# Optimization experiments

Measured on AMD Instinct MI355X. Metric: run time of the kernel, lower is better.

## Reference

```python
import jax, jax.numpy as jnp
import numpy as np

T, TOPK = 512, 2
E, H, D = 8, 2816, 1024


def setup_inputs() -> dict:
    key = jax.random.key(0)
    k1, k2, k3, k4, k5 = jax.random.split(key, 5)
    x = jax.random.normal(k1, (T, D), dtype=jnp.float32)
    expert_indices = jax.random.randint(k2, (T, TOPK), 0, E, dtype=jnp.int64)
    w1 = jax.random.normal(k3, (E, H, D), dtype=jnp.float32)
    w2 = jax.random.normal(k4, (E, H, D), dtype=jnp.float32)
    w3 = jax.random.normal(k5, (E, H, D), dtype=jnp.float32)
    return {"x": x, "expert_indices": expert_indices, "w1": w1, "w2": w2, "w3": w3}


def reference(x, expert_indices, w1, w2, w3):
    # Math identical to: silu(x @ w1[e].T) * (x @ w3[e].T) @ w2[e] for e = expert_indices[t, a].
    # Computed densely over all experts (GEMM-friendly), then gathered per token,
    # which avoids materializing [T, a, H, D] gathered weight tensors.
    h1 = jax.nn.silu(jnp.einsum('ti,ehi->teh', x, w1))   # [T, E, H]
    h3 = jnp.einsum('ti,ehi->teh', x, w3)                # [T, E, H]
    out_all = jnp.einsum('teh,ehi->tei', h1 * h3, w2)    # [T, E, D]
    # gather the top_k selected experts per token -> [T, TOPK, D]
    idx = expert_indices[:, :, None]                     # [T, a, 1]
    expert_outs = jnp.take_along_axis(out_all, idx, axis=1)
    return expert_outs
```

## Files before the change

kernel.cpp:

```cpp
#include <hip/hip_runtime.h>


#define NEXP 8
#define HDIM 2816
#define DDIM 1024
#define NPAIR 1024

typedef unsigned int uint;
typedef unsigned short ushort;
typedef __attribute__((ext_vector_type(8))) short bf16x8;
typedef __attribute__((ext_vector_type(4))) float fvec4;
typedef __attribute__((ext_vector_type(4))) uint uvec4;
typedef __attribute__((ext_vector_type(2))) uint uvec2;

__device__ __forceinline__ ushort f2bf(float f) {
    uint u = __builtin_bit_cast(uint, f);
    u += 0x7fff + ((u >> 16) & 1);
    return (ushort)(u >> 16);
}
__device__ __forceinline__ uint pack2(float lo, float hi) {
    return (uint)f2bf(lo) | ((uint)f2bf(hi) << 16);
}

__global__ __launch_bounds__(1024) void route_kernel(const int* __restrict__ idx,
                                                     int* __restrict__ counts,
                                                     int* __restrict__ lists) {
    int p = threadIdx.x;
    if (p < NEXP) counts[p] = 0;
    __syncthreads();
    int e = idx[p];
    int pos = atomicAdd(&counts[e], 1);
    lists[e * NPAIR + pos] = p;
}

#define LDA1 36

__global__ __launch_bounds__(512) void h_mfma(const float* __restrict__ x,
                       const float* __restrict__ w1,
                       const float* __restrict__ w3,
                       const int* __restrict__ counts,
                       const int* __restrict__ lists,
                       ushort* __restrict__ hb) {
    const int e = blockIdx.x;
    const int cnt = counts[e];
    const int m0 = blockIdx.z * 128;
    if (m0 >= cnt) return;
    const int h0 = blockIdx.y * 64;

    __shared__ ushort sA[128 * LDA1];
    __shared__ ushort sB1[64 * LDA1];
    __shared__ ushort sB3[64 * LDA1];
    __shared__ int sTok[128];
    __shared__ int sPairS[128];

    const int tid = threadIdx.x;
    if (tid < 128) {
        int m = m0 + tid;
        int mc = (m < cnt) ? m : (cnt - 1);
        int p = lists[e * NPAIR + mc];
        sTok[tid] = p >> 1;
        sPairS[tid] = (m < cnt) ? p : -1;
    }
    __syncthreads();

    const int w = tid >> 6;
    const int lane = tid & 63;
    const int l16 = lane & 15;
    const int quad = lane >> 4;

    const int arow = tid >> 3;
    const int ac4  = tid & 7;

    fvec4 acc1[4], acc3[4];
    #pragma unroll
    for (int i = 0; i < 4; ++i) { acc1[i] = (fvec4)0.f; acc3[i] = (fvec4)0.f; }

    const float* w1e = w1 + (size_t)e * HDIM * DDIM + (size_t)h0 * DDIM;
    const float* w3e = w3 + (size_t)e * HDIM * DDIM + (size_t)h0 * DDIM;
    const float* xr0 = x + (size_t)sTok[arow] * DDIM + ac4 * 4;
    const float* xr1 = x + (size_t)sTok[arow + 64] * DDIM + ac4 * 4;
    const float* wr1 = w1e + (size_t)arow * DDIM + ac4 * 4;
    const float* wr3 = w3e + (size_t)arow * DDIM + ac4 * 4;

    fvec4 va0, va1, vb1, vb3;
    va0 = *(const fvec4*)(xr0);
    va1 = *(const fvec4*)(xr1);
    vb1 = *(const fvec4*)(wr1);
    vb3 = *(const fvec4*)(wr3);

    for (int k0 = 0; k0 < DDIM; k0 += 32) {
        __syncthreads();
        {
            uvec2 t;
            t = (uvec2){ pack2(va0[0], va0[1]), pack2(va0[2], va0[3]) };
            *(uvec2*)&sA[arow * LDA1 + ac4 * 4] = t;
            t = (uvec2){ pack2(va1[0], va1[1]), pack2(va1[2], va1[3]) };
            *(uvec2*)&sA[(arow + 64) * LDA1 + ac4 * 4] = t;
            t = (uvec2){ pack2(vb1[0], vb1[1]), pack2(vb1[2], vb1[3]) };
            *(uvec2*)&sB1[arow * LDA1 + ac4 * 4] = t;
            t = (uvec2){ pack2(vb3[0], vb3[1]), pack2(vb3[2], vb3[3]) };
            *(uvec2*)&sB3[arow * LDA1 + ac4 * 4] = t;
        }
        __syncthreads();

        int kn = (k0 + 32 < DDIM) ? (k0 + 32) : k0;
        va0 = *(const fvec4*)(xr0 + kn);
        va1 = *(const fvec4*)(xr1 + kn);
        vb1 = *(const fvec4*)(wr1 + kn);
        vb3 = *(const fvec4*)(wr3 + kn);

        bf16x8 af = *(const bf16x8*)&sA[(w * 16 + l16) * LDA1 + quad * 8];
        #pragma unroll
        for (int ni = 0; ni < 4; ++ni) {
            bf16x8 b1 = *(const bf16x8*)&sB1[(ni * 16 + l16) * LDA1 + quad * 8];
            bf16x8 b3 = *(const bf16x8*)&sB3[(ni * 16 + l16) * LDA1 + quad * 8];
            acc1[ni] = __builtin_amdgcn_mfma_f32_16x16x32_bf16(af, b1, acc1[ni], 0, 0, 0);
            acc3[ni] = __builtin_amdgcn_mfma_f32_16x16x32_bf16(af, b3, acc3[ni], 0, 0, 0);
        }
    }

    #pragma unroll
    for (int r = 0; r < 4; ++r) {
        int m = w * 16 + quad * 4 + r;
        int p = sPairS[m];
        if (p >= 0) {
            size_t base = (size_t)p * HDIM + h0;
            #pragma unroll
            for (int ni = 0; ni < 4; ++ni) {
                float a = acc1[ni][r];
                float g = acc3[ni][r];
                float s = a / (1.f + __expf(-a)) * g;
                hb[base + ni * 16 + l16] = f2bf(s);
            }
        }
    }
}

#define LDA2 68

__global__ __launch_bounds__(512) void out_mfma(const float* __restrict__ w2,
                         const int* __restrict__ counts,
                         const int* __restrict__ lists,
                         const ushort* __restrict__ hb,
                         float* __restrict__ out) {
    const int e = blockIdx.x;
    const int cnt = counts[e];
    const int mb = blockIdx.z >> 2;
    const int sk = blockIdx.z & 3;
    const int m0 = mb * 128;
    if (m0 >= cnt) return;
    const int n0 = blockIdx.y * 64;
    const int kbase = sk * (HDIM / 4);

    __shared__ ushort sA[128 * LDA2];
    __shared__ ushort sB[64 * LDA2];
    __shared__ int sPairC[128];
    __shared__ int sPairS[128];

    const int tid = threadIdx.x;
    if (tid < 128) {
        int m = m0 + tid;
        int mc = (m < cnt) ? m : (cnt - 1);
        int p = lists[e * NPAIR + mc];
        sPairC[tid] = p;
        sPairS[tid] = (m < cnt) ? p : -1;
    }
    __syncthreads();

    const int w = tid >> 6;
    const int lane = tid & 63;
    const int l16 = lane & 15;
    const int quad = lane >> 4;

    const int arow = tid >> 3;
    const int ac   = tid & 7;
    const int kp   = tid >> 4;
    const int n4   = tid & 15;

    fvec4 acc[4];
    #pragma unroll
    for (int i = 0; i < 4; ++i) acc[i] = (fvec4)0.f;

    const float* w2e = w2 + (size_t)e * HDIM * DDIM + n0;
    const ushort* ha0 = hb + (size_t)sPairC[arow] * HDIM + ac * 8;
    const ushort* ha1 = hb + (size_t)sPairC[arow + 64] * HDIM + ac * 8;
    const float* wk0 = w2e + (size_t)(kbase + 2 * kp) * DDIM + n4 * 4;

    uvec4 va0, va1;
    fvec4 fa, fb;
    va0 = *(const uvec4*)(ha0 + kbase);
    va1 = *(const uvec4*)(ha1 + kbase);
    fa = *(const fvec4*)(wk0);
    fb = *(const fvec4*)(wk0 + DDIM);

    const int NCH = (HDIM / 4) / 64;
    for (int kc = 0; kc < NCH; ++kc) {
        __syncthreads();
        *(uvec4*)&sA[arow * LDA2 + ac * 8] = va0;
        *(uvec4*)&sA[(arow + 64) * LDA2 + ac * 8] = va1;
        #pragma unroll
        for (int j = 0; j < 4; ++j)
            *(uint*)&sB[(n4 * 4 + j) * LDA2 + kp * 2] = pack2(fa[j], fb[j]);
        __syncthreads();

        int kcn = (kc + 1 < NCH) ? (kc + 1) : kc;
        int koff = kcn * 64;
        va0 = *(const uvec4*)(ha0 + kbase + koff);
        va1 = *(const uvec4*)(ha1 + kbase + koff);
        fa = *(const fvec4*)(wk0 + (size_t)koff * DDIM);
        fb = *(const fvec4*)(wk0 + (size_t)(koff + 1) * DDIM);

        #pragma unroll
        for (int kk = 0; kk < 64; kk += 32) {
            bf16x8 af = *(const bf16x8*)&sA[(w * 16 + l16) * LDA2 + kk + quad * 8];
            #pragma unroll
            for (int ni = 0; ni < 4; ++ni) {
                bf16x8 bf = *(const bf16x8*)&sB[(ni * 16 + l16) * LDA2 + kk + quad * 8];
                acc[ni] = __builtin_amdgcn_mfma_f32_16x16x32_bf16(af, bf, acc[ni], 0, 0, 0);
            }
        }
    }

    #pragma unroll
    for (int r = 0; r < 4; ++r) {
        int m = w * 16 + quad * 4 + r;
        int p = sPairS[m];
        if (p >= 0) {
            #pragma unroll
            for (int ni = 0; ni < 4; ++ni)
                atomicAdd(&out[(size_t)p * DDIM + n0 + ni * 16 + l16], acc[ni][r]);
        }
    }
}

extern "C" void kernel_launch(void* const* d_in, const int* in_sizes, int n_in,
                              void* d_out, int out_size, void* d_ws, size_t ws_size,
                              hipStream_t stream) {
    const float* x   = (const float*)d_in[0];
    const int*   idx = (const int*)d_in[1];
    const float* w1  = (const float*)d_in[2];
    const float* w2  = (const float*)d_in[3];
    const float* w3  = (const float*)d_in[4];
    float* out = (float*)d_out;

    char* ws = (char*)d_ws;
    int*    counts = (int*)ws;
    int*    lists  = (int*)(ws + 1024);
    ushort* hbuf   = (ushort*)(ws + 65536);

    hipMemsetAsync(out, 0, (size_t)out_size * sizeof(float), stream);
    route_kernel<<<1, NPAIR, 0, stream>>>(idx, counts, lists);
    h_mfma<<<dim3(NEXP, HDIM / 64, NPAIR / 128), 512, 0, stream>>>(
        x, w1, w3, counts, lists, hbuf);
    out_mfma<<<dim3(NEXP, DDIM / 64, (NPAIR / 128) * 4), 512, 0, stream>>>(
        w2, counts, lists, hbuf, out);
}
```

Baseline: 322.9 us.

## Double-buffer weight tiles in LDS and load activation fragments directly from global

Both GEMM kernels drop the LDS staging of the A operand (gathered x rows or hidden rows). Each wave now loads its MFMA A fragments straight from global memory into registers. Weight tiles are staged as bf16 in double-buffered LDS with a 64-wide K chunk and a two-chunk-deep register prefetch, so only one barrier is needed per chunk instead of two. Launch bounds now request 3 blocks per CU. The aim is to cut barrier stalls and LDS traffic and overlap global loads with MFMA work, at the cost of more registers and A loads that are less coalesced.

```diff
diff --git a/kernel.cpp b/kernel.cpp
--- a/kernel.cpp
+++ b/kernel.cpp
@@ -11,7 +11,6 @@
 typedef __attribute__((ext_vector_type(8))) short bf16x8;
 typedef __attribute__((ext_vector_type(4))) float fvec4;
 typedef __attribute__((ext_vector_type(4))) uint uvec4;
-typedef __attribute__((ext_vector_type(2))) uint uvec2;
 
 __device__ __forceinline__ ushort f2bf(float f) {
     uint u = __builtin_bit_cast(uint, f);
@@ -20,6 +19,19 @@
 }
 __device__ __forceinline__ uint pack2(float lo, float hi) {
     return (uint)f2bf(lo) | ((uint)f2bf(hi) << 16);
+}
+__device__ __forceinline__ uvec4 pack8(fvec4 a, fvec4 b) {
+    uvec4 v;
+    v.x = pack2(a.x, a.y); v.y = pack2(a.z, a.w);
+    v.z = pack2(b.x, b.y); v.w = pack2(b.z, b.w);
+    return v;
+}
+
+__device__ __forceinline__ void wg_sync_lds() {
+    __builtin_amdgcn_sched_barrier(0);
+    asm volatile("s_waitcnt lgkmcnt(0)" ::: "memory");
+    __builtin_amdgcn_s_barrier();
+    __builtin_amdgcn_sched_barrier(0);
 }
 
 __global__ __launch_bounds__(1024) void route_kernel(const int* __restrict__ idx,
@@ -33,9 +45,10 @@
     lists[e * NPAIR + pos] = p;
 }
 
-#define LDA1 36
-
-__global__ __launch_bounds__(512) void h_mfma(const float* __restrict__ x,
+#define LDB 68
+#define NCH1 (DDIM / 64)
+
+__global__ __launch_bounds__(512, 3) void h_mfma(const float* __restrict__ x,
                        const float* __restrict__ w1,
                        const float* __restrict__ w3,
                        const int* __restrict__ counts,
@@ -47,9 +60,8 @@
     if (m0 >= cnt) return;
     const int h0 = blockIdx.y * 64;
 
-    __shared__ ushort sA[128 * LDA1];
-    __shared__ ushort sB1[64 * LDA1];
-    __shared__ ushort sB3[64 * LDA1];
+    __shared__ ushort sB1[2][64 * LDB];
+    __shared__ ushort sB3[2][64 * LDB];
     __shared__ int sTok[128];
     __shared__ int sPairS[128];
 
@@ -61,62 +73,73 @@
         sTok[tid] = p >> 1;
         sPairS[tid] = (m < cnt) ? p : -1;
     }
-    __syncthreads();
 
     const int w = tid >> 6;
     const int lane = tid & 63;
     const int l16 = lane & 15;
     const int quad = lane >> 4;
 
-    const int arow = tid >> 3;
-    const int ac4  = tid & 7;
+    const int brow = tid >> 3;
+    const int bc = (tid & 7) * 8;
+    const float* pB1 = w1 + (size_t)e * HDIM * DDIM + (size_t)(h0 + brow) * DDIM + bc;
+    const float* pB3 = w3 + (size_t)e * HDIM * DDIM + (size_t)(h0 + brow) * DDIM + bc;
+
+    fvec4 pf[2][4];
+
+#define P1_ISSUE(S, KC) do { \
+    const float* q1 = pB1 + (KC) * 64; \
+    const float* q3 = pB3 + (KC) * 64; \
+    pf[S][0] = *(const fvec4*)q1;  pf[S][1] = *(const fvec4*)(q1 + 4); \
+    pf[S][2] = *(const fvec4*)q3;  pf[S][3] = *(const fvec4*)(q3 + 4); \
+} while (0)
+
+#define P1_STAGE(S, B) do { \
+    *(uvec4*)&sB1[B][brow * LDB + bc] = pack8(pf[S][0], pf[S][1]); \
+    *(uvec4*)&sB3[B][brow * LDB + bc] = pack8(pf[S][2], pf[S][3]); \
+} while (0)
+
+    P1_ISSUE(0, 0);
+    P1_ISSUE(1, 1);
+    wg_sync_lds();
+    const float* xA = x + (size_t)sTok[w * 16 + l16] * DDIM + quad * 8;
 
     fvec4 acc1[4], acc3[4];
     #pragma unroll
     for (int i = 0; i < 4; ++i) { acc1[i] = (fvec4)0.f; acc3[i] = (fvec4)0.f; }
 
-    const float* w1e = w1 + (size_t)e * HDIM * DDIM + (size_t)h0 * DDIM;
-    const float* w3e = w3 + (size_t)e * HDIM * DDIM + (size_t)h0 * DDIM;
-    const float* xr0 = x + (size_t)sTok[arow] * DDIM + ac4 * 4;
-    const float* xr1 = x + (size_t)sTok[arow + 64] * DDIM + ac4 * 4;
-    const float* wr1 = w1e + (size_t)arow * DDIM + ac4 * 4;
-    const float* wr3 = w3e + (size_t)arow * DDIM + ac4 * 4;
-
-    fvec4 va0, va1, vb1, vb3;
-    va0 = *(const fvec4*)(xr0);
-    va1 = *(const fvec4*)(xr1);
-    vb1 = *(const fvec4*)(wr1);
-    vb3 = *(const fvec4*)(wr3);
-
-    for (int k0 = 0; k0 < DDIM; k0 += 32) {
-        __syncthreads();
-        {
-            uvec2 t;
-            t = (uvec2){ pack2(va0[0], va0[1]), pack2(va0[2], va0[3]) };
-            *(uvec2*)&sA[arow * LDA1 + ac4 * 4] = t;
-            t = (uvec2){ pack2(va1[0], va1[1]), pack2(va1[2], va1[3]) };
-            *(uvec2*)&sA[(arow + 64) * LDA1 + ac4 * 4] = t;
-            t = (uvec2){ pack2(vb1[0], vb1[1]), pack2(vb1[2], vb1[3]) };
-            *(uvec2*)&sB1[arow * LDA1 + ac4 * 4] = t;
-            t = (uvec2){ pack2(vb3[0], vb3[1]), pack2(vb3[2], vb3[3]) };
-            *(uvec2*)&sB3[arow * LDA1 + ac4 * 4] = t;
-        }
-        __syncthreads();
-
-        int kn = (k0 + 32 < DDIM) ? (k0 + 32) : k0;
-        va0 = *(const fvec4*)(xr0 + kn);
-        va1 = *(const fvec4*)(xr1 + kn);
-        vb1 = *(const fvec4*)(wr1 + kn);
-        vb3 = *(const fvec4*)(wr3 + kn);
-
-        bf16x8 af = *(const bf16x8*)&sA[(w * 16 + l16) * LDA1 + quad * 8];
-        #pragma unroll
-        for (int ni = 0; ni < 4; ++ni) {
-            bf16x8 b1 = *(const bf16x8*)&sB1[(ni * 16 + l16) * LDA1 + quad * 8];
-            bf16x8 b3 = *(const bf16x8*)&sB3[(ni * 16 + l16) * LDA1 + quad * 8];
-            acc1[ni] = __builtin_amdgcn_mfma_f32_16x16x32_bf16(af, b1, acc1[ni], 0, 0, 0);
-            acc3[ni] = __builtin_amdgcn_mfma_f32_16x16x32_bf16(af, b3, acc3[ni], 0, 0, 0);
-        }
+    P1_STAGE(0, 0);
+    wg_sync_lds();
+
+#define P1_BODY(T, CUR) do { \
+    const int kA = (T) * 64; \
+    fvec4 a0 = *(const fvec4*)(xA + kA); \
+    fvec4 a1 = *(const fvec4*)(xA + kA + 4); \
+    fvec4 a2 = *(const fvec4*)(xA + kA + 32); \
+    fvec4 a3 = *(const fvec4*)(xA + kA + 36); \
+    if ((T) + 2 < NCH1) P1_ISSUE(CUR, (T) + 2); \
+    bf16x8 af0 = __builtin_bit_cast(bf16x8, pack8(a0, a1)); \
+    bf16x8 af1 = __builtin_bit_cast(bf16x8, pack8(a2, a3)); \
+    _Pragma("unroll") \
+    for (int ni = 0; ni < 4; ++ni) { \
+        const int ro = (ni * 16 + l16) * LDB + quad * 8; \
+        bf16x8 b10 = *(const bf16x8*)&sB1[CUR][ro]; \
+        bf16x8 b30 = *(const bf16x8*)&sB3[CUR][ro]; \
+        bf16x8 b11 = *(const bf16x8*)&sB1[CUR][ro + 32]; \
+        bf16x8 b31 = *(const bf16x8*)&sB3[CUR][ro + 32]; \
+        acc1[ni] = __builtin_amdgcn_mfma_f32_16x16x32_bf16(af0, b10, acc1[ni], 0, 0, 0); \
+        acc3[ni] = __builtin_amdgcn_mfma_f32_16x16x32_bf16(af0, b30, acc3[ni], 0, 0, 0); \
+        acc1[ni] = __builtin_amdgcn_mfma_f32_16x16x32_bf16(af1, b11, acc1[ni], 0, 0, 0); \
+        acc3[ni] = __builtin_amdgcn_mfma_f32_16x16x32_bf16(af1, b31, acc3[ni], 0, 0, 0); \
+    } \
+    if ((T) + 1 < NCH1) { \
+        P1_STAGE(CUR ^ 1, CUR ^ 1); \
+        wg_sync_lds(); \
+    } \
+} while (0)
+
+    for (int t = 0; t < NCH1; t += 2) {
+        P1_BODY(t, 0);
+        P1_BODY(t + 1, 1);
     }
 
     #pragma unroll
@@ -136,9 +159,10 @@
     }
 }
 
-#define LDA2 68
-
-__global__ __launch_bounds__(512) void out_mfma(const float* __restrict__ w2,
+#define LDB2 68
+#define NCH2 ((HDIM / 4) / 64)
+
+__global__ __launch_bounds__(512, 3) void out_mfma(const float* __restrict__ w2,
                          const int* __restrict__ counts,
                          const int* __restrict__ lists,
                          const ushort* __restrict__ hb,
@@ -152,8 +176,7 @@
     const int n0 = blockIdx.y * 64;
     const int kbase = sk * (HDIM / 4);
 
-    __shared__ ushort sA[128 * LDA2];
-    __shared__ ushort sB[64 * LDA2];
+    __shared__ ushort sB[2][64 * LDB2];
     __shared__ int sPairC[128];
     __shared__ int sPairS[128];
 
@@ -165,60 +188,65 @@
         sPairC[tid] = p;
         sPairS[tid] = (m < cnt) ? p : -1;
     }
-    __syncthreads();
 
     const int w = tid >> 6;
     const int lane = tid & 63;
     const int l16 = lane & 15;
     const int quad = lane >> 4;
-
-    const int arow = tid >> 3;
-    const int ac   = tid & 7;
-    const int kp   = tid >> 4;
-    const int n4   = tid & 15;
+    const int kp = tid >> 4;
+    const int n4 = tid & 15;
+
+    const float* pW = w2 + (size_t)e * HDIM * DDIM
+                         + (size_t)(kbase + 2 * kp) * DDIM + n0 + n4 * 4;
+
+    fvec4 pw[2][2];
+
+#define P2_ISSUE(S, KC) do { \
+    const float* q = pW + (size_t)(KC) * 64 * DDIM; \
+    pw[S][0] = *(const fvec4*)q; \
+    pw[S][1] = *(const fvec4*)(q + DDIM); \
+} while (0)
+
+#define P2_STAGE(S, B) do { \
+    _Pragma("unroll") \
+    for (int j = 0; j < 4; ++j) \
+        *(uint*)&sB[B][(n4 * 4 + j) * LDB2 + kp * 2] = pack2(pw[S][0][j], pw[S][1][j]); \
+} while (0)
+
+    P2_ISSUE(0, 0);
+    P2_ISSUE(1, 1);
+    wg_sync_lds();
+    const ushort* pA = hb + (size_t)sPairC[w * 16 + l16] * HDIM + kbase + quad * 8;
 
     fvec4 acc[4];
     #pragma unroll
     for (int i = 0; i < 4; ++i) acc[i] = (fvec4)0.f;
 
-    const float* w2e = w2 + (size_t)e * HDIM * DDIM + n0;
-    const ushort* ha0 = hb + (size_t)sPairC[arow] * HDIM + ac * 8;
-    const ushort* ha1 = hb + (size_t)sPairC[arow + 64] * HDIM + ac * 8;
-    const float* wk0 = w2e + (size_t)(kbase + 2 * kp) * DDIM + n4 * 4;
-
-    uvec4 va0, va1;
-    fvec4 fa, fb;
-    va0 = *(const uvec4*)(ha0 + kbase);
-    va1 = *(const uvec4*)(ha1 + kbase);
-    fa = *(const fvec4*)(wk0);
-    fb = *(const fvec4*)(wk0 + DDIM);
-
-    const int NCH = (HDIM / 4) / 64;
-    for (int kc = 0; kc < NCH; ++kc) {
-        __syncthreads();
-        *(uvec4*)&sA[arow * LDA2 + ac * 8] = va0;
-        *(uvec4*)&sA[(arow + 64) * LDA2 + ac * 8] = va1;
-        #pragma unroll
-        for (int j = 0; j < 4; ++j)
-            *(uint*)&sB[(n4 * 4 + j) * LDA2 + kp * 2] = pack2(fa[j], fb[j]);
-        __syncthreads();
-
-        int kcn = (kc + 1 < NCH) ? (kc + 1) : kc;
-        int koff = kcn * 64;
-        va0 = *(const uvec4*)(ha0 + kbase + koff);
-        va1 = *(const uvec4*)(ha1 + kbase + koff);
-        fa = *(const fvec4*)(wk0 + (size_t)koff * DDIM);
-        fb = *(const fvec4*)(wk0 + (size_t)(koff + 1) * DDIM);
-
-        #pragma unroll
-        for (int kk = 0; kk < 64; kk += 32) {
-            bf16x8 af = *(const bf16x8*)&sA[(w * 16 + l16) * LDA2 + kk + quad * 8];
-            #pragma unroll
-            for (int ni = 0; ni < 4; ++ni) {
-                bf16x8 bf = *(const bf16x8*)&sB[(ni * 16 + l16) * LDA2 + kk + quad * 8];
-                acc[ni] = __builtin_amdgcn_mfma_f32_16x16x32_bf16(af, bf, acc[ni], 0, 0, 0);
-            }
-        }
+    P2_STAGE(0, 0);
+    wg_sync_lds();
+
+#define P2_BODY(T, CUR) do { \
+    const int kA = (T) * 64; \
+    bf16x8 af0 = *(const bf16x8*)(pA + kA); \
+    bf16x8 af1 = *(const bf16x8*)(pA + kA + 32); \
+    if ((T) + 2 < NCH2) P2_ISSUE(CUR, (T) + 2); \
+    _Pragma("unroll") \
+    for (int ni = 0; ni < 4; ++ni) { \
+        const int ro = (ni * 16 + l16) * LDB2 + quad * 8; \
+        bf16x8 b0 = *(const bf16x8*)&sB[CUR][ro]; \
+        bf16x8 b1 = *(const bf16x8*)&sB[CUR][ro + 32]; \
+        acc[ni] = __builtin_amdgcn_mfma_f32_16x16x32_bf16(af0, b0, acc[ni], 0, 0, 0); \
+        acc[ni] = __builtin_amdgcn_mfma_f32_16x16x32_bf16(af1, b1, acc[ni], 0, 0, 0); \
+    } \
+    if ((T) + 1 < NCH2) { \
+        P2_STAGE(CUR ^ 1, CUR ^ 1); \
+        wg_sync_lds(); \
+    } \
+} while (0)
+
+    for (int t = 0; t < NCH2; t += 2) {
+        P2_BODY(t, 0);
+        if (t + 1 < NCH2) P2_BODY(t + 1, 1);
     }
 
     #pragma unroll
```

Result: slower. 330.1 us (+2.2%).
